# Performance work log

Measured on AMD Instinct MI355X. Metric: run time of the kernel, lower is better.

Reference implementation:

```python
import jax, jax.numpy as jnp
import numpy as np

N_NODES = 100000
N_EDGES = 1600000
D_FEAT = 128
HIDDEN = 128
HEADS = 4
OUT_C = HIDDEN // HEADS  # 32
N_CLASSES = 10
N_GRAPHS = 64
NEG_SLOPE = 0.2


def glorot(key, shape, fan_in, fan_out):
    s = jnp.sqrt(6.0 / (fan_in + fan_out))
    return jax.random.uniform(key, shape, minval=-s, maxval=s, dtype=jnp.float32)


def setup_inputs() -> dict:
    key = jax.random.key(0)
    ks = jax.random.split(key, 24)
    x = jax.random.normal(ks[0], (N_NODES, D_FEAT), dtype=jnp.float32)
    src = jax.random.randint(ks[1], (N_EDGES,), 0, N_NODES, dtype=jnp.int32)
    off = jax.random.randint(ks[2], (N_EDGES,), 1, N_NODES, dtype=jnp.int32)
    dst = ((src + off) % N_NODES).astype(jnp.int32)  # guarantees no self-loops
    edge_index = jnp.stack([src, dst], axis=0)
    batch = jnp.sort(jax.random.randint(ks[3], (N_NODES,), 0, N_GRAPHS, dtype=jnp.int32))
    inp = {"x": x, "edge_index": edge_index, "batch": batch}
    # GATConv layer params: W [in, H*C] (lin_l == lin_r), att_l/att_r [H, C], bias [H*C]
    ins = [D_FEAT, HIDDEN, HIDDEN]
    for i in range(3):
        k = 4 + 4 * i
        inp[f"W{i+1}"] = glorot(ks[k], (ins[i], HEADS * OUT_C), ins[i], HEADS * OUT_C)
        inp[f"al{i+1}"] = glorot(ks[k + 1], (HEADS, OUT_C), HEADS * OUT_C, 1)
        inp[f"ar{i+1}"] = glorot(ks[k + 2], (HEADS, OUT_C), HEADS * OUT_C, 1)
        inp[f"b{i+1}"] = jnp.zeros((HEADS * OUT_C,), jnp.float32)
    inp["lin1_w"] = glorot(ks[16], (HIDDEN, HIDDEN), HIDDEN, HIDDEN)
    inp["lin1_b"] = jnp.zeros((HIDDEN,), jnp.float32)
    inp["lin2_w"] = glorot(ks[17], (HIDDEN, N_CLASSES), HIDDEN, N_CLASSES)
    inp["lin2_b"] = jnp.zeros((N_CLASSES,), jnp.float32)
    return inp


def gat_layer(x, src, dst, W, att_l, att_r, bias):
    n = x.shape[0]
    H, C = att_l.shape
    xw = (x @ W).reshape(n, H, C)                       # Theta x
    al = jnp.einsum('nhc,hc->nh', xw, att_l)
    ar = jnp.einsum('nhc,hc->nh', xw, att_r)
    loop = jnp.arange(n, dtype=src.dtype)
    s = jnp.concatenate([src, loop])                    # add self-loops
    d = jnp.concatenate([dst, loop])
    logits = jax.nn.leaky_relu(al[s] + ar[d], NEG_SLOPE)  # [E+N, H]
    m = jax.ops.segment_max(logits, d, num_segments=n)    # segment softmax over dst
    e = jnp.exp(logits - m[d])
    z = jax.ops.segment_sum(e, d, num_segments=n)
    alpha = e / z[d]
    msg = xw[s] * alpha[:, :, None]                     # [E+N, H, C]
    out = jax.ops.segment_sum(msg, d, num_segments=n)   # scatter-add aggregate
    return out.reshape(n, H * C) + bias


def reference(x, edge_index, batch,
              W1, al1, ar1, b1, W2, al2, ar2, b2, W3, al3, ar3, b3,
              lin1_w, lin1_b, lin2_w, lin2_b):
    src, dst = edge_index[0], edge_index[1]
    h = jax.nn.relu(gat_layer(x, src, dst, W1, al1, ar1, b1))
    h = jax.nn.relu(gat_layer(h, src, dst, W2, al2, ar2, b2))
    h = jax.nn.relu(gat_layer(h, src, dst, W3, al3, ar3, b3))
    last = h
    # global mean pool over graphs in the batch
    s = jax.ops.segment_sum(h, batch, num_segments=N_GRAPHS)
    cnt = jax.ops.segment_sum(jnp.ones((h.shape[0],), h.dtype), batch, num_segments=N_GRAPHS)
    pooled = s / jnp.maximum(cnt, 1.0)[:, None]
    g = jax.nn.relu(pooled @ lin1_w + lin1_b)           # dropout inactive (eval)
    logits = g @ lin2_w + lin2_b
    return (jax.nn.log_softmax(logits, axis=-1), last)
```

## Files before the change

kernel.cpp:

```cpp
#include <hip/hip_runtime.h>
#include <math.h>


#define LRELU(x) ((x) > 0.f ? (x) : 0.2f*(x))
#define SH 8
#define TILE 4096
#define EPT 16
#define PSL 64

typedef __attribute__((ext_vector_type(8))) short s16x8;
typedef __attribute__((ext_vector_type(4))) float f32x4;

__device__ inline unsigned short f2bf(float f){
  unsigned u = __float_as_uint(f);
  u += 0x7fff + ((u >> 16) & 1);
  return (unsigned short)(u >> 16);
}

__global__ void k_init(int* __restrict__ bcnt, float* __restrict__ psum,
                       const float* __restrict__ W0, const float* __restrict__ W1,
                       const float* __restrict__ W2, unsigned short* __restrict__ wt3){
  int t = threadIdx.x;
  if (blockIdx.x == 0){
    bcnt[t] = 0; bcnt[256 + t] = 0;
    for (int i = t; i < 8192; i += 256) psum[i] = 0.f;
    return;
  }
  int e = ((int)blockIdx.x - 1)*256 + t;
  int layer = e >> 14, rem = e & 16383;
  int k = rem >> 7, nn = rem & 127;
  const float* Ws = layer == 0 ? W0 : (layer == 1 ? W1 : W2);
  wt3[layer*16384 + nn*128 + k] = f2bf(Ws[k*128 + nn]);
}

template<bool BF16IN>
__device__ __forceinline__ void gemm_body(
    unsigned short* Xl, unsigned short* Cl,
    const void* __restrict__ Xv, const unsigned short* __restrict__ Wtg,
    const float* __restrict__ attl, const float* __restrict__ attr,
    unsigned short* __restrict__ XW, float* __restrict__ AL, float* __restrict__ AR,
    int n, int tlo, int thi, int bid, int gstride)
{
  int t = threadIdx.x;
  int lane = t & 63, w = t >> 6;
  int l15 = lane & 15, quad = lane >> 4;
  int r_ = t >> 2, seg = t & 3;
  const unsigned short* Bp0 = Wtg + (w*32 + l15)*128 + quad*8;
  const unsigned short* Bp1 = Bp0 + 16*128;
  s16x8 b0r[4], b1r[4];
  #pragma unroll
  for (int ks = 0; ks < 4; ks++){
    b0r[ks] = *(const s16x8*)(Bp0 + ks*32);
    b1r[ks] = *(const s16x8*)(Bp1 + ks*32);
  }
  for (int tile = tlo + bid; tile < thi; tile += gstride){
    int row0 = tile << 6;
    {
      int grow = row0 + r_;
      unsigned short* dp = &Xl[r_*136 + seg*32];
      if (grow < n){
        if (BF16IN){
          const uint4* gp = (const uint4*)((const unsigned short*)Xv + (size_t)grow*128 + seg*32);
          #pragma unroll
          for (int i = 0; i < 4; i++) ((uint4*)dp)[i] = gp[i];
        } else {
          const float4* gp = (const float4*)((const float*)Xv + (size_t)grow*128 + seg*32);
          #pragma unroll
          for (int i = 0; i < 8; i++){
            float4 v = gp[i];
            ((unsigned*)dp)[i*2]   = (unsigned)f2bf(v.x) | ((unsigned)f2bf(v.y) << 16);
            ((unsigned*)dp)[i*2+1] = (unsigned)f2bf(v.z) | ((unsigned)f2bf(v.w) << 16);
          }
        }
      } else {
        #pragma unroll
        for (int i = 0; i < 4; i++) ((uint4*)dp)[i] = make_uint4(0,0,0,0);
      }
    }
    __syncthreads();
    f32x4 acc[4][2];
    #pragma unroll
    for (int rt = 0; rt < 4; rt++){ acc[rt][0] = (f32x4){0,0,0,0}; acc[rt][1] = (f32x4){0,0,0,0}; }
    #pragma unroll
    for (int ks = 0; ks < 4; ks++){
      #pragma unroll
      for (int rt = 0; rt < 4; rt++){
        s16x8 a = *(const s16x8*)&Xl[(rt*16 + l15)*136 + ks*32 + quad*8];
        acc[rt][0] = __builtin_amdgcn_mfma_f32_16x16x32_bf16(a, b0r[ks], acc[rt][0], 0, 0, 0);
        acc[rt][1] = __builtin_amdgcn_mfma_f32_16x16x32_bf16(a, b1r[ks], acc[rt][1], 0, 0, 0);
      }
    }
    #pragma unroll
    for (int rt = 0; rt < 4; rt++)
      #pragma unroll
      for (int c2 = 0; c2 < 2; c2++)
        #pragma unroll
        for (int r = 0; r < 4; r++)
          Cl[(rt*16 + quad*4 + r)*136 + w*32 + c2*16 + l15] = f2bf(acc[rt][c2][r]);
    __syncthreads();
    {
      int grow = row0 + r_;
      if (grow < n){
        const unsigned short* sp = &Cl[r_*136 + seg*32];
        uint4 uu[4];
        #pragma unroll
        for (int i = 0; i < 4; i++) uu[i] = ((const uint4*)sp)[i];
        unsigned short* gx = XW + (size_t)grow*128 + seg*32;
        #pragma unroll
        for (int i = 0; i < 4; i++) ((uint4*)gx)[i] = uu[i];
        const unsigned* up = (const unsigned*)uu;
        const float4* alp = (const float4*)(attl + seg*32);
        const float4* arp = (const float4*)(attr + seg*32);
        float pl = 0.f, pr = 0.f;
        #pragma unroll
        for (int i = 0; i < 8; i++){
          unsigned ua = up[i*2], ub = up[i*2+1];
          float x0 = __uint_as_float(ua << 16);
          float x1 = __uint_as_float(ua & 0xffff0000u);
          float x2 = __uint_as_float(ub << 16);
          float x3 = __uint_as_float(ub & 0xffff0000u);
          float4 av = alp[i];
          float4 rv = arp[i];
          pl += x0*av.x + x1*av.y + x2*av.z + x3*av.w;
          pr += x0*rv.x + x1*rv.y + x2*rv.z + x3*rv.w;
        }
        AL[grow*4 + seg] = pl;
        AR[grow*4 + seg] = pr;
      }
    }
  }
}

template<bool BF16IN>
__global__ __launch_bounds__(256) void k_gemm(
    const void* __restrict__ Xv, const unsigned short* __restrict__ Wtg,
    const float* __restrict__ attl, const float* __restrict__ attr,
    unsigned short* __restrict__ XW, float* __restrict__ AL, float* __restrict__ AR, int n)
{
  __shared__ unsigned short Xl[64*136];
  __shared__ unsigned short Cl[64*136];
  int ntiles = (n + 63) >> 6;
  gemm_body<BF16IN>(Xl, Cl, Xv, Wtg, attl, attr, XW, AL, AR, n,
                    0, ntiles, blockIdx.x, gridDim.x);
}

__global__ __launch_bounds__(256) void k_fuse1(
    const int* __restrict__ dst, int* __restrict__ bcnt, int E, int nparts,
    const float* __restrict__ X, const unsigned short* __restrict__ Wtg,
    const float* __restrict__ attl, const float* __restrict__ attr,
    unsigned short* __restrict__ XW, float* __restrict__ AL, float* __restrict__ AR,
    int n, int T1)
{
  __shared__ unsigned short Xl[64*136];
  __shared__ unsigned short Cl[64*136];
  if ((int)blockIdx.x < nparts){
    int* lh = (int*)Xl;
    int t = threadIdx.x;
    for (int j = t; j < 512; j += 256) lh[j] = 0;
    __syncthreads();
    int base = blockIdx.x * TILE;
    int lim = min(base + TILE, E);
    for (int e = base + t; e < lim; e += 256)
      atomicAdd(&lh[dst[e] >> SH], 1);
    __syncthreads();
    for (int j = t; j < 512; j += 256){
      int v = lh[j];
      if (v) atomicAdd(&bcnt[j], v);
    }
    return;
  }
  gemm_body<false>(Xl, Cl, X, Wtg, attl, attr, XW, AL, AR, n,
                   0, T1, (int)blockIdx.x - nparts, (int)gridDim.x - nparts);
}

__global__ __launch_bounds__(256) void k_bscan(const int* __restrict__ bcnt,
    int* __restrict__ bstart, int* __restrict__ bfill, int NB, int E,
    const int* __restrict__ batch, int* __restrict__ gstart, int n){
  int t = threadIdx.x;
  if (blockIdx.x == 1){
    int g = t;
    if (g > 64) return;
    int lo = 0, hi = n;
    while (lo < hi){
      int mid = (lo + hi) >> 1;
      if (batch[mid] < g) lo = mid + 1; else hi = mid;
    }
    gstart[g] = lo;
    return;
  }
  __shared__ int c[512];
  __shared__ int ps[256];
  for (int j = t; j < 512; j += 256) c[j] = (j < NB) ? bcnt[j] : 0;
  __syncthreads();
  int b0 = 2*t;
  int v0 = c[b0], v1 = c[b0+1];
  int ts = v0 + v1;
  ps[t] = ts; __syncthreads();
  for (int off = 1; off < 256; off <<= 1){
    int x = (t >= off) ? ps[t-off] : 0; __syncthreads();
    ps[t] += x; __syncthreads();
  }
  int pre = ps[t] - ts;
  if (b0   < NB){ bstart[b0]   = pre;    bfill[b0]   = pre; }
  if (b0+1 < NB){ bstart[b0+1] = pre+v0; bfill[b0+1] = pre+v0; }
  if (t == 0) bstart[NB] = E;
}

__global__ __launch_bounds__(256) void k_part2(const int* __restrict__ src,
    const int* __restrict__ dst, int* __restrict__ bfill,
    int2* __restrict__ tmp, int E,
    const float* __restrict__ X, const unsigned short* __restrict__ Wtg,
    const float* __restrict__ attl, const float* __restrict__ attr,
    unsigned short* __restrict__ XW, float* __restrict__ AL, float* __restrict__ AR,
    int n, int T1, int T2){
  __shared__ __align__(16) char smem[40960];
  int nparts = (E + TILE - 1) / TILE;
  int t = threadIdx.x;
  if ((int)blockIdx.x >= nparts){
    unsigned short* Xl = (unsigned short*)smem;
    unsigned short* Cl = (unsigned short*)(smem + 17408);
    gemm_body<false>(Xl, Cl, X, Wtg, attl, attr, XW, AL, AR, n,
                     T1, T2, (int)blockIdx.x - nparts, (int)gridDim.x - nparts);
    return;
  }
  int2* reorder = (int2*)smem;
  int* lhist  = (int*)(smem + 32768);
  int* lscan  = (int*)(smem + 34816);
  int* lgbase = (int*)(smem + 36864);
  int* ps     = (int*)(smem + 38912);
  int tb = blockIdx.x * TILE;
  int tilecnt = min(TILE, E - tb);
  for (int j = t; j < 512; j += 256) lhist[j] = 0;
  __syncthreads();
  int ss[EPT], dd[EPT], rk[EPT];
  #pragma unroll
  for (int i = 0; i < EPT; i++){
    int e = tb + t + i*256;
    if (e < E){
      ss[i] = src[e]; dd[i] = dst[e];
      rk[i] = atomicAdd(&lhist[dd[i] >> SH], 1);
    }
  }
  __syncthreads();
  int b0 = 2*t;
  int v0 = lhist[b0], v1 = lhist[b0+1];
  int ts = v0 + v1;
  ps[t] = ts; __syncthreads();
  for (int off = 1; off < 256; off <<= 1){
    int x = (t >= off) ? ps[t-off] : 0; __syncthreads();
    ps[t] += x; __syncthreads();
  }
  int pre = ps[t] - ts;
  int ex0 = pre, ex1 = pre + v0;
  lscan[b0] = ex0; lscan[b0+1] = ex1;
  if (v0 > 0){ int gb = atomicAdd(&bfill[b0],   v0); lgbase[b0]   = gb - ex0; }
  if (v1 > 0){ int gb = atomicAdd(&bfill[b0+1], v1); lgbase[b0+1] = gb - ex1; }
  __syncthreads();
  #pragma unroll
  for (int i = 0; i < EPT; i++){
    int e = tb + t + i*256;
    if (e < E){
      int b = dd[i] >> SH;
      reorder[lscan[b] + rk[i]] = make_int2(ss[i], dd[i]);
    }
  }
  __syncthreads();
  for (int j = t; j < tilecnt; j += 256){
    int2 p = reorder[j];
    tmp[lgbase[p.y >> SH] + j] = p;
  }
}

__global__ __launch_bounds__(256) void k_csr2(const int2* __restrict__ tmp,
    const int* __restrict__ bstart, int* __restrict__ rp, int* __restrict__ col,
    int n, int E,
    const float* __restrict__ X, const unsigned short* __restrict__ Wtg,
    const float* __restrict__ attl, const float* __restrict__ attr,
    unsigned short* __restrict__ XW, float* __restrict__ AL, float* __restrict__ AR,
    int T2){
  __shared__ __align__(16) char smem[34816];
  int NB = (n + 255) >> SH;
  int t = threadIdx.x;
  if ((int)blockIdx.x >= NB){
    unsigned short* Xl = (unsigned short*)smem;
    unsigned short* Cl = (unsigned short*)(smem + 17408);
    int ntiles = (n + 63) >> 6;
    gemm_body<false>(Xl, Cl, X, Wtg, attl, attr, XW, AL, AR, n,
                     T2, ntiles, (int)blockIdx.x - NB, (int)gridDim.x - NB);
    return;
  }
  int* lcnt = (int*)smem;
  int* sc   = (int*)(smem + 1024);
  int b = blockIdx.x;
  int node0 = b << SH;
  int ncnt = min(256, n - node0);
  int be = bstart[b], ee = bstart[b+1];
  lcnt[t] = 0;
  __syncthreads();
  for (int e = be + t; e < ee; e += 256)
    atomicAdd(&lcnt[tmp[e].y - node0], 1);
  __syncthreads();
  int v = lcnt[t];
  sc[t] = v;
  __syncthreads();
  for (int off = 1; off < 256; off <<= 1){
    int x = (t >= off) ? sc[t-off] : 0;
    __syncthreads();
    sc[t] += x;
    __syncthreads();
  }
  int start = be + sc[t] - v;
  lcnt[t] = start;
  if (t < ncnt) rp[node0 + t] = start;
  if (t == 0 && node0 + ncnt == n) rp[n] = E;
  __syncthreads();
  for (int e = be + t; e < ee; e += 256){
    int2 p = tmp[e];
    int pos = atomicAdd(&lcnt[p.y - node0], 1);
    col[pos] = p.x;
  }
}

template<bool BF16OUT>
__global__ __launch_bounds__(256) void k_attn(
    const unsigned short* __restrict__ XW, const float* __restrict__ AL, const float* __restrict__ AR,
    const int* __restrict__ rp, const int* __restrict__ col,
    const float* __restrict__ bias, void* __restrict__ OUT, int dbase, int nmax)
{
  __shared__ int   ws[4][512];
  __shared__ float arsh[4][4][4];
  int wv = threadIdx.x >> 6;
  int lane = threadIdx.x & 63;
  int r = lane & 15, g = lane >> 4, h2 = r >> 2;
  int d0 = dbase + (blockIdx.x*4 + wv)*4;
  if (d0 >= nmax) return;
  int d = d0 + g;
  bool valid = d < nmax;
  int dc = valid ? d : nmax-1;
  int rs = rp[dc];
  int re = valid ? rp[dc+1] : rs;
  float4 ard4 = ((const float4*)AR)[dc];
  if (r == 0) *(float4*)&arsh[wv][g][0] = ard4;
  float4 ald4 = ((const float4*)AL)[dc];
  float alh = h2==0?ald4.x : h2==1?ald4.y : h2==2?ald4.z : ald4.w;
  float arh = h2==0?ard4.x : h2==1?ard4.y : h2==2?ard4.z : ard4.w;
  float tse = alh + arh;
  float eself = __expf(fmaxf(tse, 0.2f*tse));
  const uint4* XW4 = (const uint4*)XW;
  float acc[8];
  {
    uint4 v = XW4[(size_t)dc*16 + r];
    acc[0] = eself * __uint_as_float(v.x << 16);
    acc[1] = eself * __uint_as_float(v.x & 0xffff0000u);
    acc[2] = eself * __uint_as_float(v.y << 16);
    acc[3] = eself * __uint_as_float(v.y & 0xffff0000u);
    acc[4] = eself * __uint_as_float(v.z << 16);
    acc[5] = eself * __uint_as_float(v.z & 0xffff0000u);
    acc[6] = eself * __uint_as_float(v.w << 16);
    acc[7] = eself * __uint_as_float(v.w & 0xffff0000u);
  }
  int ub0 = rp[d0];
  int ubE = rp[min(d0+4, nmax)];
  int reb = valid ? re : 0x7fffffff;
  int b1 = __shfl(reb, 0, 64);
  int b2 = __shfl(reb, 16, 64);
  int b3 = __shfl(reb, 32, 64);
  int* wsw = ws[wv];
  float zacc = eself;
  for (int cb = ub0; cb < ubE; cb += 64){
    int cnt = min(64, ubE - cb);
    if (lane < cnt){
      int e = cb + lane;
      int s = col[e];
      int eg = (e >= b1) + (e >= b2) + (e >= b3);
      float4 arr = *(const float4*)&arsh[wv][eg][0];
      float4 a = ((const float4*)AL)[s];
      float t0 = a.x + arr.x, t1 = a.y + arr.y, t2 = a.z + arr.z, t3 = a.w + arr.w;
      float w0 = __expf(fmaxf(t0, 0.2f*t0));
      float w1 = __expf(fmaxf(t1, 0.2f*t1));
      float w2 = __expf(fmaxf(t2, 0.2f*t2));
      float w3 = __expf(fmaxf(t3, 0.2f*t3));
      int s4 = s << 4;
      ((int4*)&wsw[lane*8])[0] = make_int4(s4, __float_as_int(w0), s4, __float_as_int(w1));
      ((int4*)&wsw[lane*8])[1] = make_int4(s4, __float_as_int(w2), s4, __float_as_int(w3));
    }
    int jlo = max(rs - cb, 0);
    int jhi = min(re - cb, cnt);
    #pragma unroll 4
    for (int j = jlo; j < jhi; ++j){
      int2 q = *(const int2*)&wsw[j*8 + h2*2];
      float w = __int_as_float(q.y);
      uint4 u = XW4[(unsigned)(q.x + r)];
      acc[0] = fmaf(w, __uint_as_float(u.x << 16), acc[0]);
      acc[1] = fmaf(w, __uint_as_float(u.x & 0xffff0000u), acc[1]);
      acc[2] = fmaf(w, __uint_as_float(u.y << 16), acc[2]);
      acc[3] = fmaf(w, __uint_as_float(u.y & 0xffff0000u), acc[3]);
      acc[4] = fmaf(w, __uint_as_float(u.z << 16), acc[4]);
      acc[5] = fmaf(w, __uint_as_float(u.z & 0xffff0000u), acc[5]);
      acc[6] = fmaf(w, __uint_as_float(u.w << 16), acc[6]);
      acc[7] = fmaf(w, __uint_as_float(u.w & 0xffff0000u), acc[7]);
      zacc += w;
    }
  }
  float rz = 1.f / zacc;
  float4 bb0 = ((const float4*)bias)[r*2];
  float4 bb1 = ((const float4*)bias)[r*2 + 1];
  float o[8];
  o[0] = fmaf(acc[0], rz, bb0.x); o[1] = fmaf(acc[1], rz, bb0.y);
  o[2] = fmaf(acc[2], rz, bb0.z); o[3] = fmaf(acc[3], rz, bb0.w);
  o[4] = fmaf(acc[4], rz, bb1.x); o[5] = fmaf(acc[5], rz, bb1.y);
  o[6] = fmaf(acc[6], rz, bb1.z); o[7] = fmaf(acc[7], rz, bb1.w);
  #pragma unroll
  for (int i = 0; i < 8; i++) o[i] = o[i] > 0.f ? o[i] : 0.f;
  if (valid){
    if (BF16OUT){
      uint4 pk;
      pk.x = (unsigned)f2bf(o[0]) | ((unsigned)f2bf(o[1]) << 16);
      pk.y = (unsigned)f2bf(o[2]) | ((unsigned)f2bf(o[3]) << 16);
      pk.z = (unsigned)f2bf(o[4]) | ((unsigned)f2bf(o[5]) << 16);
      pk.w = (unsigned)f2bf(o[6]) | ((unsigned)f2bf(o[7]) << 16);
      ((uint4*)OUT)[(size_t)d*16 + r] = pk;
    } else {
      float4 f0; f0.x = o[0]; f0.y = o[1]; f0.z = o[2]; f0.w = o[3];
      float4 f1; f1.x = o[4]; f1.y = o[5]; f1.z = o[6]; f1.w = o[7];
      ((float4*)OUT)[(size_t)d*32 + r*2]     = f0;
      ((float4*)OUT)[(size_t)d*32 + r*2 + 1] = f1;
    }
  }
}

__global__ __launch_bounds__(128) void k_pool(const float* __restrict__ H,
                                              const int* __restrict__ gstart,
                                              float* __restrict__ psum){
  int g = blockIdx.x >> 6, slice = blockIdx.x & (PSL-1), t = threadIdx.x;
  int s0 = gstart[g], s1 = gstart[g+1];
  int cntg = s1 - s0;
  int chunk = (cntg + PSL-1) / PSL;
  int lo = s0 + slice*chunk;
  int hi = min(lo + chunk, s1);
  if (lo >= hi) return;
  float sum = 0.f;
  for (int i = lo; i < hi; i++) sum += H[(size_t)i*128 + t];
  atomicAdd(&psum[g*128 + t], sum);
}

__global__ __launch_bounds__(128) void k_mlp(const float* __restrict__ psum,
                       const int* __restrict__ gstart,
                       const float* __restrict__ w1, const float* __restrict__ b1,
                       const float* __restrict__ w2, const float* __restrict__ b2,
                       float* __restrict__ out)
{
  __shared__ float p[128];
  __shared__ float gsh[128];
  __shared__ float lg[10];
  int g = blockIdx.x, t = threadIdx.x;
  float c = fmaxf((float)(gstart[g+1] - gstart[g]), 1.f);
  p[t] = psum[g*128 + t] / c;
  __syncthreads();
  float acc = b1[t];
  for (int k = 0; k < 128; k++) acc = fmaf(p[k], w1[k*128 + t], acc);
  gsh[t] = acc > 0.f ? acc : 0.f;
  __syncthreads();
  if (t < 10){
    float a = b2[t];
    for (int k = 0; k < 128; k++) a = fmaf(gsh[k], w2[k*10 + t], a);
    lg[t] = a;
  }
  __syncthreads();
  if (t < 10){
    float mx = lg[0];
    for (int c2 = 1; c2 < 10; c2++) mx = fmaxf(mx, lg[c2]);
    float se = 0.f;
    for (int c2 = 0; c2 < 10; c2++) se += __expf(lg[c2] - mx);
    out[g*10 + t] = lg[t] - mx - logf(se);
  }
}

extern "C" void kernel_launch(void* const* d_in, const int* in_sizes, int n_in,
                              void* d_out, int out_size, void* d_ws, size_t ws_size,
                              hipStream_t stream)
{
  const float* x    = (const float*)d_in[0];
  const int* eidx   = (const int*)d_in[1];
  const int* batch  = (const int*)d_in[2];
  const float* W[3]  = {(const float*)d_in[3], (const float*)d_in[7],  (const float*)d_in[11]};
  const float* al[3] = {(const float*)d_in[4], (const float*)d_in[8],  (const float*)d_in[12]};
  const float* ar[3] = {(const float*)d_in[5], (const float*)d_in[9],  (const float*)d_in[13]};
  const float* bs[3] = {(const float*)d_in[6], (const float*)d_in[10], (const float*)d_in[14]};
  const float* l1w = (const float*)d_in[15];
  const float* l1b = (const float*)d_in[16];
  const float* l2w = (const float*)d_in[17];
  const float* l2b = (const float*)d_in[18];
  int E = in_sizes[1] / 2;
  int n = in_sizes[2];
  const int* srcp = eidx;
  const int* dstp = eidx + E;
  int NB = (n + 255) >> SH;

  char* wsp = (char*)d_ws;
  auto alloc = [&](size_t bytes){ void* p = (void*)wsp; wsp += (bytes + 255) & ~(size_t)255; return p; };
  unsigned short* xw   = (unsigned short*)alloc((size_t)n*128*2);
  unsigned short* hbuf = (unsigned short*)alloc((size_t)n*128*2);
  float* ALb  = (float*)alloc((size_t)n*4*4);
  float* ARb  = (float*)alloc((size_t)n*4*4);
  int* rp     = (int*)alloc((size_t)(n+1)*4);
  int* col    = (int*)alloc((size_t)E*4);
  int2* tmp   = (int2*)alloc((size_t)E*8);
  int* bcnt   = (int*)alloc(512*4);
  int* bstart = (int*)alloc(513*4);
  int* bfill  = (int*)alloc(512*4);
  float* psum = (float*)alloc(64*128*4);
  int* gstart = (int*)alloc(65*4);
  unsigned short* wt3 = (unsigned short*)alloc(3*16384*2);

  float* outlog = (float*)d_out;
  float* h3     = (float*)d_out + 64*10;

  int nparts = (E + TILE - 1) / TILE;
  int ntiles = (n + 63) >> 6;
  int T1 = ntiles / 6;
  int T2 = T1 + (int)((long long)(ntiles - T1) * 54 / 100);
  int G1 = T1 > 0 ? T1 : 1;
  int G2 = (T2 - T1) > 0 ? (T2 - T1) : 1;
  int G3 = (ntiles - T2) > 0 ? (ntiles - T2) : 1;

  k_init<<<193, 256, 0, stream>>>(bcnt, psum, W[0], W[1], W[2], wt3);
  k_fuse1<<<nparts + G1, 256, 0, stream>>>(dstp, bcnt, E, nparts,
                                           x, wt3, al[0], ar[0], xw, ALb, ARb, n, T1);
  k_bscan<<<2, 256, 0, stream>>>(bcnt, bstart, bfill, NB, E, batch, gstart, n);
  k_part2<<<nparts + G2, 256, 0, stream>>>(srcp, dstp, bfill, tmp, E,
                                           x, wt3, al[0], ar[0], xw, ALb, ARb, n, T1, T2);
  k_csr2 <<<NB + G3, 256, 0, stream>>>(tmp, bstart, rp, col, n, E,
                                       x, wt3, al[0], ar[0], xw, ALb, ARb, T2);

  int ablk = (n + 15) / 16;
  k_attn<true><<<ablk, 256, 0, stream>>>(xw, ALb, ARb, rp, col, bs[0], hbuf, 0, n);
  k_gemm<true><<<1024, 256, 0, stream>>>(hbuf, wt3 + 16384, al[1], ar[1], xw, ALb, ARb, n);
  k_attn<true><<<ablk, 256, 0, stream>>>(xw, ALb, ARb, rp, col, bs[1], hbuf, 0, n);
  k_gemm<true><<<1024, 256, 0, stream>>>(hbuf, wt3 + 32768, al[2], ar[2], xw, ALb, ARb, n);
  k_attn<false><<<ablk, 256, 0, stream>>>(xw, ALb, ARb, rp, col, bs[2], h3, 0, n);

  k_pool<<<64*PSL, 128, 0, stream>>>(h3, gstart, psum);
  k_mlp <<<64, 128, 0, stream>>>(psum, gstart, l1w, l1b, l2w, l2b, outlog);
}
```

Baseline: 494.4 us.

## Split attention aggregation into two head-pair passes over half the features

The attention kernel now covers only two of the four heads (64 features) per launch, using 8 lanes per destination node and 8 nodes per wavefront, and runs twice per layer with a head-pair index. The aim is to halve the gathered XW working set per pass so that source rows are more likely to hit in cache, and to raise the number of destinations handled per wave. In exchange, the CSR column indices, AL values and edge walk are each read twice per layer, and there are extra kernel launches.

```diff
diff --git a/kernel.cpp b/kernel.cpp
--- a/kernel.cpp
+++ b/kernel.cpp
@@ -322,34 +322,34 @@
 }
 
 template<bool BF16OUT>
-__global__ __launch_bounds__(256) void k_attn(
+__global__ __launch_bounds__(256) void k_attn2(
     const unsigned short* __restrict__ XW, const float* __restrict__ AL, const float* __restrict__ AR,
     const int* __restrict__ rp, const int* __restrict__ col,
-    const float* __restrict__ bias, void* __restrict__ OUT, int dbase, int nmax)
+    const float* __restrict__ bias, void* __restrict__ OUT, int nmax, int hp)
 {
-  __shared__ int   ws[4][512];
-  __shared__ float arsh[4][4][4];
+  __shared__ int   ws[4][256];
+  __shared__ float arsh[4][8][2];
   int wv = threadIdx.x >> 6;
   int lane = threadIdx.x & 63;
-  int r = lane & 15, g = lane >> 4, h2 = r >> 2;
-  int d0 = dbase + (blockIdx.x*4 + wv)*4;
+  int r = lane & 7, g = lane >> 3, hh = r >> 2;
+  int d0 = (blockIdx.x*4 + wv)*8;
   if (d0 >= nmax) return;
   int d = d0 + g;
   bool valid = d < nmax;
   int dc = valid ? d : nmax-1;
   int rs = rp[dc];
   int re = valid ? rp[dc+1] : rs;
-  float4 ard4 = ((const float4*)AR)[dc];
-  if (r == 0) *(float4*)&arsh[wv][g][0] = ard4;
-  float4 ald4 = ((const float4*)AL)[dc];
-  float alh = h2==0?ald4.x : h2==1?ald4.y : h2==2?ald4.z : ald4.w;
-  float arh = h2==0?ard4.x : h2==1?ard4.y : h2==2?ard4.z : ard4.w;
+  float2 ar2 = ((const float2*)AR)[(size_t)dc*2 + hp];
+  if (r == 0) *(float2*)&arsh[wv][g][0] = ar2;
+  float2 al2 = ((const float2*)AL)[(size_t)dc*2 + hp];
+  float alh = hh ? al2.y : al2.x;
+  float arh = hh ? ar2.y : ar2.x;
   float tse = alh + arh;
   float eself = __expf(fmaxf(tse, 0.2f*tse));
   const uint4* XW4 = (const uint4*)XW;
   float acc[8];
   {
-    uint4 v = XW4[(size_t)dc*16 + r];
+    uint4 v = XW4[(size_t)dc*16 + hp*8 + r];
     acc[0] = eself * __uint_as_float(v.x << 16);
     acc[1] = eself * __uint_as_float(v.x & 0xffff0000u);
     acc[2] = eself * __uint_as_float(v.y << 16);
@@ -360,11 +360,15 @@
     acc[7] = eself * __uint_as_float(v.w & 0xffff0000u);
   }
   int ub0 = rp[d0];
-  int ubE = rp[min(d0+4, nmax)];
+  int ubE = rp[min(d0+8, nmax)];
   int reb = valid ? re : 0x7fffffff;
   int b1 = __shfl(reb, 0, 64);
-  int b2 = __shfl(reb, 16, 64);
-  int b3 = __shfl(reb, 32, 64);
+  int b2 = __shfl(reb, 8, 64);
+  int b3 = __shfl(reb, 16, 64);
+  int b4 = __shfl(reb, 24, 64);
+  int b5 = __shfl(reb, 32, 64);
+  int b6 = __shfl(reb, 40, 64);
+  int b7 = __shfl(reb, 48, 64);
   int* wsw = ws[wv];
   float zacc = eself;
   for (int cb = ub0; cb < ubE; cb += 64){
@@ -372,23 +376,20 @@
     if (lane < cnt){
       int e = cb + lane;
       int s = col[e];
-      int eg = (e >= b1) + (e >= b2) + (e >= b3);
-      float4 arr = *(const float4*)&arsh[wv][eg][0];
-      float4 a = ((const float4*)AL)[s];
-      float t0 = a.x + arr.x, t1 = a.y + arr.y, t2 = a.z + arr.z, t3 = a.w + arr.w;
+      int eg = (e>=b1)+(e>=b2)+(e>=b3)+(e>=b4)+(e>=b5)+(e>=b6)+(e>=b7);
+      float2 arr = *(const float2*)&arsh[wv][eg][0];
+      float2 a2 = ((const float2*)AL)[(size_t)s*2 + hp];
+      float t0 = a2.x + arr.x, t1 = a2.y + arr.y;
       float w0 = __expf(fmaxf(t0, 0.2f*t0));
       float w1 = __expf(fmaxf(t1, 0.2f*t1));
-      float w2 = __expf(fmaxf(t2, 0.2f*t2));
-      float w3 = __expf(fmaxf(t3, 0.2f*t3));
-      int s4 = s << 4;
-      ((int4*)&wsw[lane*8])[0] = make_int4(s4, __float_as_int(w0), s4, __float_as_int(w1));
-      ((int4*)&wsw[lane*8])[1] = make_int4(s4, __float_as_int(w2), s4, __float_as_int(w3));
+      int s4 = (s << 4) + (hp << 3);
+      ((int4*)&wsw[lane*4])[0] = make_int4(s4, __float_as_int(w0), s4, __float_as_int(w1));
     }
     int jlo = max(rs - cb, 0);
     int jhi = min(re - cb, cnt);
     #pragma unroll 4
     for (int j = jlo; j < jhi; ++j){
-      int2 q = *(const int2*)&wsw[j*8 + h2*2];
+      int2 q = *(const int2*)&wsw[j*4 + hh*2];
       float w = __int_as_float(q.y);
       uint4 u = XW4[(unsigned)(q.x + r)];
       acc[0] = fmaf(w, __uint_as_float(u.x << 16), acc[0]);
@@ -403,8 +404,8 @@
     }
   }
   float rz = 1.f / zacc;
-  float4 bb0 = ((const float4*)bias)[r*2];
-  float4 bb1 = ((const float4*)bias)[r*2 + 1];
+  float4 bb0 = ((const float4*)bias)[hp*16 + r*2];
+  float4 bb1 = ((const float4*)bias)[hp*16 + r*2 + 1];
   float o[8];
   o[0] = fmaf(acc[0], rz, bb0.x); o[1] = fmaf(acc[1], rz, bb0.y);
   o[2] = fmaf(acc[2], rz, bb0.z); o[3] = fmaf(acc[3], rz, bb0.w);
@@ -419,12 +420,12 @@
       pk.y = (unsigned)f2bf(o[2]) | ((unsigned)f2bf(o[3]) << 16);
       pk.z = (unsigned)f2bf(o[4]) | ((unsigned)f2bf(o[5]) << 16);
       pk.w = (unsigned)f2bf(o[6]) | ((unsigned)f2bf(o[7]) << 16);
-      ((uint4*)OUT)[(size_t)d*16 + r] = pk;
+      ((uint4*)OUT)[(size_t)d*16 + hp*8 + r] = pk;
     } else {
       float4 f0; f0.x = o[0]; f0.y = o[1]; f0.z = o[2]; f0.w = o[3];
       float4 f1; f1.x = o[4]; f1.y = o[5]; f1.z = o[6]; f1.w = o[7];
-      ((float4*)OUT)[(size_t)d*32 + r*2]     = f0;
-      ((float4*)OUT)[(size_t)d*32 + r*2 + 1] = f1;
+      ((float4*)OUT)[(size_t)d*32 + hp*16 + r*2]     = f0;
+      ((float4*)OUT)[(size_t)d*32 + hp*16 + r*2 + 1] = f1;
     }
   }
 }
@@ -533,12 +534,15 @@
   k_csr2 <<<NB + G3, 256, 0, stream>>>(tmp, bstart, rp, col, n, E,
                                        x, wt3, al[0], ar[0], xw, ALb, ARb, T2);
 
-  int ablk = (n + 15) / 16;
-  k_attn<true><<<ablk, 256, 0, stream>>>(xw, ALb, ARb, rp, col, bs[0], hbuf, 0, n);
+  int ablk2 = (n + 31) / 32;
+  k_attn2<true><<<ablk2, 256, 0, stream>>>(xw, ALb, ARb, rp, col, bs[0], hbuf, n, 0);
+  k_attn2<true><<<ablk2, 256, 0, stream>>>(xw, ALb, ARb, rp, col, bs[0], hbuf, n, 1);
   k_gemm<true><<<1024, 256, 0, stream>>>(hbuf, wt3 + 16384, al[1], ar[1], xw, ALb, ARb, n);
-  k_attn<true><<<ablk, 256, 0, stream>>>(xw, ALb, ARb, rp, col, bs[1], hbuf, 0, n);
+  k_attn2<true><<<ablk2, 256, 0, stream>>>(xw, ALb, ARb, rp, col, bs[1], hbuf, n, 0);
+  k_attn2<true><<<ablk2, 256, 0, stream>>>(xw, ALb, ARb, rp, col, bs[1], hbuf, n, 1);
   k_gemm<true><<<1024, 256, 0, stream>>>(hbuf, wt3 + 32768, al[2], ar[2], xw, ALb, ARb, n);
-  k_attn<false><<<ablk, 256, 0, stream>>>(xw, ALb, ARb, rp, col, bs[2], h3, 0, n);
+  k_attn2<false><<<ablk2, 256, 0, stream>>>(xw, ALb, ARb, rp, col, bs[2], h3, n, 0);
+  k_attn2<false><<<ablk2, 256, 0, stream>>>(xw, ALb, ARb, rp, col, bs[2], h3, n, 1);
 
   k_pool<<<64*PSL, 128, 0, stream>>>(h3, gstart, psum);
   k_mlp <<<64, 128, 0, stream>>>(psum, gstart, l1w, l1b, l2w, l2b, outlog);
```

New measurement: 542.2 us. 9.7% more time.
